# Kernel tuning notes

Measured on AMD Instinct MI355X. Metric: run time of the kernel, lower is better.

## Reference

```python
import jax, jax.numpy as jnp
import numpy as np

D_MODEL = 1024
N_HEADS = 16
HEAD_DIM = D_MODEL // N_HEADS
SCALE = float(np.sqrt(HEAD_DIM))


def setup_inputs() -> dict:
    key = jax.random.key(0)
    ks = jax.random.split(key, 12)
    B, S, D = 4, 2048, D_MODEL
    std = 1.0 / np.sqrt(D)
    inp = {
        "query": jax.random.normal(ks[0], (B, S, D), jnp.float32),
        "key": jax.random.normal(ks[1], (B, S, D), jnp.float32),
        "value": jax.random.normal(ks[2], (B, S, D), jnp.float32),
        "wq_w": jax.random.normal(ks[3], (D, D), jnp.float32) * std,
        "wq_b": jnp.zeros((D,), jnp.float32),
        "wk_w": jax.random.normal(ks[4], (D, D), jnp.float32) * std,
        "wk_b": jnp.zeros((D,), jnp.float32),
        "wv_w": jax.random.normal(ks[5], (D, D), jnp.float32) * std,
        "wv_b": jnp.zeros((D,), jnp.float32),
        "fc_w": jax.random.normal(ks[6], (D, D), jnp.float32) * std,
        "fc_b": jnp.zeros((D,), jnp.float32),
    }
    return inp


def reference(query, key, value, wq_w, wq_b, wk_w, wk_b, wv_w, wv_b, fc_w, fc_b):
    B, S, D = query.shape
    H, Hd = N_HEADS, HEAD_DIM
    # QKV projections (torch Linear: x @ W.T + b)
    Q = query @ wq_w.T + wq_b
    K = key @ wk_w.T + wk_b
    V = value @ wv_w.T + wv_b
    # [B, H, S, Hd]
    Q = Q.reshape(B, S, H, Hd).transpose(0, 2, 1, 3)
    K = K.reshape(B, S, H, Hd).transpose(0, 2, 1, 3)
    V = V.reshape(B, S, H, Hd).transpose(0, 2, 1, 3)
    energy = jnp.einsum("bhqd,bhkd->bhqk", Q, K) / SCALE
    attention = jax.nn.softmax(energy, axis=-1)  # dropout=0 (eval)
    weighted = jnp.einsum("bhqk,bhkd->bhqd", attention, V)
    weighted = weighted.transpose(0, 2, 1, 3).reshape(B, S, D)
    output = weighted @ fc_w.T + fc_b
    return (output, attention)
```

## Files before the change

kernel.cpp:

```cpp
#include <hip/hip_runtime.h>
#include <hip/hip_bf16.h>
#include <math.h>

typedef __attribute__((ext_vector_type(8))) short short8;
typedef __attribute__((ext_vector_type(4))) short short4v;
typedef __attribute__((ext_vector_type(4))) float float4v;
typedef __attribute__((ext_vector_type(2))) unsigned int uint2v;

#define GLD_LDS(g, l) __builtin_amdgcn_global_load_lds( \
    (const __attribute__((address_space(1))) void*)(g), \
    (__attribute__((address_space(3))) void*)(l), 16, 0, 0)

__device__ __forceinline__ short f2bf(float x) {
  __hip_bfloat16 h = __float2bfloat16(x);
  return __builtin_bit_cast(short, h);
}

__global__ __launch_bounds__(256) void cast3(
    const float4v* __restrict__ in0, const float4v* __restrict__ in1,
    const float4v* __restrict__ in2,
    short4v* __restrict__ o0, short4v* __restrict__ o1, short4v* __restrict__ o2,
    int n4)
{
  const float4v* in = blockIdx.y == 0 ? in0 : blockIdx.y == 1 ? in1 : in2;
  short4v* out = blockIdx.y == 0 ? o0 : blockIdx.y == 1 ? o1 : o2;
  int i = blockIdx.x * 256 + threadIdx.x;
  if (i < n4) {
    float4v v = in[i];
    short4v o;
    o[0] = f2bf(v[0]); o[1] = f2bf(v[1]); o[2] = f2bf(v[2]); o[3] = f2bf(v[3]);
    out[i] = o;
  }
}

__global__ __launch_bounds__(256) void cast4(
    const float4v* __restrict__ in0, const float4v* __restrict__ in1,
    const float4v* __restrict__ in2, const float4v* __restrict__ in3,
    short4v* __restrict__ o0, short4v* __restrict__ o1,
    short4v* __restrict__ o2, short4v* __restrict__ o3,
    int n4)
{
  const float4v* in = blockIdx.y == 0 ? in0 : blockIdx.y == 1 ? in1
                    : blockIdx.y == 2 ? in2 : in3;
  short4v* out = blockIdx.y == 0 ? o0 : blockIdx.y == 1 ? o1
               : blockIdx.y == 2 ? o2 : o3;
  int i = blockIdx.x * 256 + threadIdx.x;
  if (i < n4) {
    float4v v = in[i];
    short4v o;
    o[0] = f2bf(v[0]); o[1] = f2bf(v[1]); o[2] = f2bf(v[2]); o[3] = f2bf(v[3]);
    out[i] = o;
  }
}

template<int MODE>
__global__ __launch_bounds__(256) void gemm_bt(
    const short* __restrict__ A, const short* __restrict__ B,
    const float* __restrict__ bias, void* __restrict__ Cv,
    int M, int N, int K)
{
  __shared__ short As[2][128 * 64];
  __shared__ short Bs[2][128 * 64];
  const int tid = threadIdx.x;
  const int w = tid >> 6, lane = tid & 63;
  const int g = lane >> 4, cc = lane & 15;
  const int m0 = blockIdx.x * 128, n0 = blockIdx.y * 128;
  const int wr = (w >> 1) * 64, wc = (w & 1) * 64;

  float4v acc[4][4];
#pragma unroll
  for (int mi = 0; mi < 4; ++mi)
#pragma unroll
    for (int ni = 0; ni < 4; ++ni)
      acc[mi][ni] = (float4v){0.f, 0.f, 0.f, 0.f};

  const int cbase0 = w * 64;
  const int row_l[4] = {(cbase0 + lane) >> 3, (256 + cbase0 + lane) >> 3,
                        (512 + cbase0 + lane) >> 3, (768 + cbase0 + lane) >> 3};
  const int col_l = (lane & 7) * 8;

  auto stage = [&](int buf, int k0) {
#pragma unroll
    for (int i = 0; i < 4; ++i) {
      int cbase = i * 256 + cbase0;
      GLD_LDS(A + (long)(m0 + row_l[i]) * K + k0 + col_l, &As[buf][cbase * 8]);
      GLD_LDS(B + (long)(n0 + row_l[i]) * K + k0 + col_l, &Bs[buf][cbase * 8]);
    }
  };
  auto compute = [&](int buf) {
#pragma unroll
    for (int ks = 0; ks < 2; ++ks) {
      short8 af[4], bfr[4];
#pragma unroll
      for (int mi = 0; mi < 4; ++mi)
        af[mi] = *(const short8*)&As[buf][(wr + mi * 16 + cc) * 64 + ks * 32 + g * 8];
#pragma unroll
      for (int ni = 0; ni < 4; ++ni)
        bfr[ni] = *(const short8*)&Bs[buf][(wc + ni * 16 + cc) * 64 + ks * 32 + g * 8];
#pragma unroll
      for (int mi = 0; mi < 4; ++mi)
#pragma unroll
        for (int ni = 0; ni < 4; ++ni)
          acc[mi][ni] = __builtin_amdgcn_mfma_f32_16x16x32_bf16(
              af[mi], bfr[ni], acc[mi][ni], 0, 0, 0);
    }
  };

  stage(0, 0);
  __syncthreads();
#pragma unroll 1
  for (int k0 = 0; k0 < K; k0 += 128) {
    stage(1, k0 + 64);
    compute(0);
    __syncthreads();
    if (k0 + 128 < K) stage(0, k0 + 128);
    compute(1);
    __syncthreads();
  }

#pragma unroll
  for (int mi = 0; mi < 4; ++mi) {
#pragma unroll
    for (int ni = 0; ni < 4; ++ni) {
      int mb = m0 + wr + mi * 16 + g * 4;
      int nn = n0 + wc + ni * 16 + cc;
      float4v v = acc[mi][ni];
      if constexpr (MODE == 0) {
        float bb = bias[nn];
        __hip_bfloat16* C = (__hip_bfloat16*)Cv;
#pragma unroll
        for (int r = 0; r < 4; ++r)
          C[(long)(mb + r) * N + nn] = __float2bfloat16(v[r] + bb);
      } else if constexpr (MODE == 1) {
        __hip_bfloat16* C = (__hip_bfloat16*)Cv;
        long base = (long)(nn >> 11) * 2097152 + (nn & 2047);
#pragma unroll
        for (int r = 0; r < 4; ++r)
          C[(long)(mb + r) * 2048 + base] = __float2bfloat16(v[r] + bias[mb + r]);
      } else {
        float bb = bias[nn];
        float* C = (float*)Cv;
#pragma unroll
        for (int r = 0; r < 4; ++r)
          C[(long)(mb + r) * N + nn] = v[r] + bb;
      }
    }
  }
}

__global__ __launch_bounds__(256) void attn_fwd(
    const short* __restrict__ Qb, const short* __restrict__ Kb,
    const short* __restrict__ VTb, float* __restrict__ attn_out,
    __hip_bfloat16* __restrict__ Wout)
{
  __shared__ short plds[4][32][72];
  const int S = 2048, D = 1024;
  const int bid = blockIdx.x;
  const int x = bid >> 7, r = bid & 127;
  const int bh = x * 8 + (r & 7), qi = r >> 3;
  const int b = bh >> 4, h = bh & 15;
  const int tid = threadIdx.x, w = tid >> 6, lane = tid & 63;
  const int g = lane >> 4, cc = lane & 15;
  const int q0 = qi * 128 + w * 32;

  const short* Qp = Qb + (long)b * S * D + h * 64;
  const short* Kp = Kb + (long)b * S * D + h * 64;
  const short* Vt = VTb + (long)bh * 64 * S;

  short8 qf[2][2];
#pragma unroll
  for (int mi = 0; mi < 2; ++mi)
#pragma unroll
    for (int ks = 0; ks < 2; ++ks)
      qf[mi][ks] = *(const short8*)(Qp + (long)(q0 + mi * 16 + cc) * D + ks * 32 + g * 8);

  float l[2] = {0.f, 0.f};
  const float C2 = 0.18033688011112042f;

#pragma unroll 1
  for (int kt = 0; kt < S; kt += 64) {
    float4v e[2][4];
#pragma unroll
    for (int mi = 0; mi < 2; ++mi)
#pragma unroll
      for (int ni = 0; ni < 4; ++ni) e[mi][ni] = (float4v){0.f, 0.f, 0.f, 0.f};
#pragma unroll
    for (int ks = 0; ks < 2; ++ks) {
      short8 kf[4];
#pragma unroll
      for (int ni = 0; ni < 4; ++ni)
        kf[ni] = *(const short8*)(Kp + (long)(kt + ni * 16 + cc) * D + ks * 32 + g * 8);
#pragma unroll
      for (int mi = 0; mi < 2; ++mi)
#pragma unroll
        for (int ni = 0; ni < 4; ++ni)
          e[mi][ni] = __builtin_amdgcn_mfma_f32_16x16x32_bf16(
              kf[ni], qf[mi][ks], e[mi][ni], 0, 0, 0);
    }
#pragma unroll
    for (int mi = 0; mi < 2; ++mi)
#pragma unroll
      for (int ni = 0; ni < 4; ++ni)
#pragma unroll
        for (int r2 = 0; r2 < 4; ++r2)
          l[mi] += __builtin_exp2f(e[mi][ni][r2] * C2);
  }
  float lrl[2];
#pragma unroll
  for (int mi = 0; mi < 2; ++mi) {
    float s = l[mi];
    s += __shfl_xor(s, 16);
    s += __shfl_xor(s, 32);
    lrl[mi] = -__log2f(s);
  }

  float4v Wacc[2][4];
#pragma unroll
  for (int mi = 0; mi < 2; ++mi)
#pragma unroll
    for (int ni = 0; ni < 4; ++ni) Wacc[mi][ni] = (float4v){0.f, 0.f, 0.f, 0.f};

  float* Arow = attn_out + (long)bh * S * S;
#pragma unroll 1
  for (int kt = 0; kt < S; kt += 64) {
    float4v e[2][4];
#pragma unroll
    for (int mi = 0; mi < 2; ++mi)
#pragma unroll
      for (int ni = 0; ni < 4; ++ni) e[mi][ni] = (float4v){0.f, 0.f, 0.f, 0.f};
#pragma unroll
    for (int ks = 0; ks < 2; ++ks) {
      short8 kf[4];
#pragma unroll
      for (int ni = 0; ni < 4; ++ni)
        kf[ni] = *(const short8*)(Kp + (long)(kt + ni * 16 + cc) * D + ks * 32 + g * 8);
#pragma unroll
      for (int mi = 0; mi < 2; ++mi)
#pragma unroll
        for (int ni = 0; ni < 4; ++ni)
          e[mi][ni] = __builtin_amdgcn_mfma_f32_16x16x32_bf16(
              kf[ni], qf[mi][ks], e[mi][ni], 0, 0, 0);
    }
#pragma unroll
    for (int mi = 0; mi < 2; ++mi) {
#pragma unroll
      for (int ni = 0; ni < 4; ++ni) {
        short4v pb;
#pragma unroll
        for (int r2 = 0; r2 < 4; ++r2)
          pb[r2] = f2bf(__builtin_exp2f(__builtin_fmaf(e[mi][ni][r2], C2, lrl[mi])));
        *(short4v*)&plds[w][mi * 16 + cc][ni * 16 + g * 4] = pb;
      }
    }
#pragma unroll
    for (int j = 0; j < 8; ++j) {
      uint2v u = *(const uint2v*)&plds[w][j * 4 + g][cc * 4];
      float4v pv4;
      pv4[0] = __builtin_bit_cast(float, u[0] << 16);
      pv4[1] = __builtin_bit_cast(float, u[0] & 0xffff0000u);
      pv4[2] = __builtin_bit_cast(float, u[1] << 16);
      pv4[3] = __builtin_bit_cast(float, u[1] & 0xffff0000u);
      __builtin_nontemporal_store(
          pv4, (float4v*)(Arow + (long)(q0 + j * 4 + g) * S + kt + cc * 4));
    }
#pragma unroll
    for (int ks = 0; ks < 2; ++ks) {
      short8 pa[2], vf[4];
#pragma unroll
      for (int mi = 0; mi < 2; ++mi)
        pa[mi] = *(const short8*)&plds[w][mi * 16 + cc][ks * 32 + g * 8];
#pragma unroll
      for (int ni = 0; ni < 4; ++ni)
        vf[ni] = *(const short8*)(Vt + (long)(ni * 16 + cc) * S + kt + ks * 32 + g * 8);
#pragma unroll
      for (int mi = 0; mi < 2; ++mi)
#pragma unroll
        for (int ni = 0; ni < 4; ++ni)
          Wacc[mi][ni] = __builtin_amdgcn_mfma_f32_16x16x32_bf16(
              pa[mi], vf[ni], Wacc[mi][ni], 0, 0, 0);
    }
  }

#pragma unroll
  for (int mi = 0; mi < 2; ++mi)
#pragma unroll
    for (int ni = 0; ni < 4; ++ni)
#pragma unroll
      for (int r2 = 0; r2 < 4; ++r2)
        Wout[(long)(b * S + q0 + mi * 16 + g * 4 + r2) * D + h * 64 + ni * 16 + cc] =
            __float2bfloat16(Wacc[mi][ni][r2]);
}

extern "C" void kernel_launch(void* const* d_in, const int* in_sizes, int n_in,
                              void* d_out, int out_size, void* d_ws, size_t ws_size,
                              hipStream_t stream) {
  const float* query = (const float*)d_in[0];
  const float* key   = (const float*)d_in[1];
  const float* value = (const float*)d_in[2];
  const float* wq_w  = (const float*)d_in[3];
  const float* wq_b  = (const float*)d_in[4];
  const float* wk_w  = (const float*)d_in[5];
  const float* wk_b  = (const float*)d_in[6];
  const float* wv_w  = (const float*)d_in[7];
  const float* wv_b  = (const float*)d_in[8];
  const float* fc_w  = (const float*)d_in[9];
  const float* fc_b  = (const float*)d_in[10];

  char* ws = (char*)d_ws;
  short* Qb  = (short*)(ws);
  short* Kb  = (short*)(ws + 16777216);
  short* VT  = (short*)(ws + 33554432);
  short* Wq  = (short*)(ws + 50331648);
  short* Wk  = (short*)(ws + 52428800);
  short* Wv  = (short*)(ws + 54525952);
  short* Wfc = (short*)(ws + 56623104);
  short* Xq  = (short*)(ws + 58720256);
  short* Xk  = (short*)(ws + 75497472);
  short* Xv  = (short*)(ws + 92274688);
  short* Wgt = Xq;

  float* out0 = (float*)d_out;
  float* attn_out = out0 + 8388608;

  cast3<<<dim3(8192, 3), 256, 0, stream>>>(
      (const float4v*)query, (const float4v*)key, (const float4v*)value,
      (short4v*)Xq, (short4v*)Xk, (short4v*)Xv, 2097152);
  cast4<<<dim3(1024, 4), 256, 0, stream>>>(
      (const float4v*)wq_w, (const float4v*)wk_w, (const float4v*)wv_w,
      (const float4v*)fc_w,
      (short4v*)Wq, (short4v*)Wk, (short4v*)Wv, (short4v*)Wfc, 262144);

  gemm_bt<0><<<dim3(64, 8), 256, 0, stream>>>(Xq, Wq, wq_b, Qb, 8192, 1024, 1024);
  gemm_bt<0><<<dim3(64, 8), 256, 0, stream>>>(Xk, Wk, wk_b, Kb, 8192, 1024, 1024);
  gemm_bt<1><<<dim3(8, 64), 256, 0, stream>>>(Wv, Xv, wv_b, VT, 1024, 8192, 1024);

  attn_fwd<<<dim3(1024), 256, 0, stream>>>(Qb, Kb, VT, attn_out,
                                           (__hip_bfloat16*)Wgt);

  gemm_bt<2><<<dim3(64, 8), 256, 0, stream>>>(Wgt, Wfc, fc_b, out0, 8192, 1024, 1024);
}
```

Measured before the change: 543.0 us.

## Halve attention rows per wave to raise occupancy and parallelism

Each wave in the attention kernel now handles 16 query rows instead of 32, and each block covers 64 rows, so the grid grows to 2048 blocks laid out as (32,64). The block-to-head swizzle is dropped. Launch bounds now request 4 blocks per CU, the LDS tile is halved, and exp2 goes through the raw amdgcn intrinsic. Fewer registers per wave and more blocks are meant to hide memory latency on the large attention-matrix writes. In exchange, K and V are loaded twice as often per computed row, which reduces reuse and L2 locality across heads.

```diff
diff --git a/kernel.cpp b/kernel.cpp
--- a/kernel.cpp
+++ b/kernel.cpp
@@ -14,6 +14,10 @@
 __device__ __forceinline__ short f2bf(float x) {
   __hip_bfloat16 h = __float2bfloat16(x);
   return __builtin_bit_cast(short, h);
+}
+
+__device__ __forceinline__ float fexp2(float x) {
+  return __builtin_amdgcn_exp2f(x);
 }
 
 __global__ __launch_bounds__(256) void cast3(
@@ -148,112 +152,91 @@
   }
 }
 
-__global__ __launch_bounds__(256) void attn_fwd(
+__global__ __launch_bounds__(256, 4) void attn_fwd(
     const short* __restrict__ Qb, const short* __restrict__ Kb,
     const short* __restrict__ VTb, float* __restrict__ attn_out,
     __hip_bfloat16* __restrict__ Wout)
 {
-  __shared__ short plds[4][32][72];
+  __shared__ short plds[4][16][72];
   const int S = 2048, D = 1024;
-  const int bid = blockIdx.x;
-  const int x = bid >> 7, r = bid & 127;
-  const int bh = x * 8 + (r & 7), qi = r >> 3;
-  const int b = bh >> 4, h = bh & 15;
+  const int bh = blockIdx.y, b = bh >> 4, h = bh & 15;
   const int tid = threadIdx.x, w = tid >> 6, lane = tid & 63;
   const int g = lane >> 4, cc = lane & 15;
-  const int q0 = qi * 128 + w * 32;
+  const int q0 = blockIdx.x * 64 + w * 16;
 
   const short* Qp = Qb + (long)b * S * D + h * 64;
   const short* Kp = Kb + (long)b * S * D + h * 64;
   const short* Vt = VTb + (long)bh * 64 * S;
 
-  short8 qf[2][2];
-#pragma unroll
-  for (int mi = 0; mi < 2; ++mi)
-#pragma unroll
-    for (int ks = 0; ks < 2; ++ks)
-      qf[mi][ks] = *(const short8*)(Qp + (long)(q0 + mi * 16 + cc) * D + ks * 32 + g * 8);
-
-  float l[2] = {0.f, 0.f};
+  short8 qf[2];
+#pragma unroll
+  for (int ks = 0; ks < 2; ++ks)
+    qf[ks] = *(const short8*)(Qp + (long)(q0 + cc) * D + ks * 32 + g * 8);
+
+  float l = 0.f;
   const float C2 = 0.18033688011112042f;
 
 #pragma unroll 1
   for (int kt = 0; kt < S; kt += 64) {
-    float4v e[2][4];
-#pragma unroll
-    for (int mi = 0; mi < 2; ++mi)
-#pragma unroll
-      for (int ni = 0; ni < 4; ++ni) e[mi][ni] = (float4v){0.f, 0.f, 0.f, 0.f};
-#pragma unroll
-    for (int ks = 0; ks < 2; ++ks) {
-      short8 kf[4];
-#pragma unroll
-      for (int ni = 0; ni < 4; ++ni)
-        kf[ni] = *(const short8*)(Kp + (long)(kt + ni * 16 + cc) * D + ks * 32 + g * 8);
-#pragma unroll
-      for (int mi = 0; mi < 2; ++mi)
-#pragma unroll
-        for (int ni = 0; ni < 4; ++ni)
-          e[mi][ni] = __builtin_amdgcn_mfma_f32_16x16x32_bf16(
-              kf[ni], qf[mi][ks], e[mi][ni], 0, 0, 0);
-    }
-#pragma unroll
-    for (int mi = 0; mi < 2; ++mi)
-#pragma unroll
-      for (int ni = 0; ni < 4; ++ni)
-#pragma unroll
-        for (int r2 = 0; r2 < 4; ++r2)
-          l[mi] += __builtin_exp2f(e[mi][ni][r2] * C2);
-  }
-  float lrl[2];
-#pragma unroll
-  for (int mi = 0; mi < 2; ++mi) {
-    float s = l[mi];
-    s += __shfl_xor(s, 16);
-    s += __shfl_xor(s, 32);
-    lrl[mi] = -__log2f(s);
-  }
-
-  float4v Wacc[2][4];
-#pragma unroll
-  for (int mi = 0; mi < 2; ++mi)
-#pragma unroll
-    for (int ni = 0; ni < 4; ++ni) Wacc[mi][ni] = (float4v){0.f, 0.f, 0.f, 0.f};
+    short8 kf[2][4];
+#pragma unroll
+    for (int ks = 0; ks < 2; ++ks)
+#pragma unroll
+      for (int ni = 0; ni < 4; ++ni)
+        kf[ks][ni] = *(const short8*)(Kp + (long)(kt + ni * 16 + cc) * D + ks * 32 + g * 8);
+    float4v e[4];
+#pragma unroll
+    for (int ni = 0; ni < 4; ++ni) e[ni] = (float4v){0.f, 0.f, 0.f, 0.f};
+#pragma unroll
+    for (int ks = 0; ks < 2; ++ks)
+#pragma unroll
+      for (int ni = 0; ni < 4; ++ni)
+        e[ni] = __builtin_amdgcn_mfma_f32_16x16x32_bf16(
+            kf[ks][ni], qf[ks], e[ni], 0, 0, 0);
+#pragma unroll
+    for (int ni = 0; ni < 4; ++ni)
+#pragma unroll
+      for (int r2 = 0; r2 < 4; ++r2)
+        l += fexp2(e[ni][r2] * C2);
+  }
+  {
+    l += __shfl_xor(l, 16);
+    l += __shfl_xor(l, 32);
+  }
+  const float lrl = -__log2f(l);
+
+  float4v Wacc[4];
+#pragma unroll
+  for (int ni = 0; ni < 4; ++ni) Wacc[ni] = (float4v){0.f, 0.f, 0.f, 0.f};
 
   float* Arow = attn_out + (long)bh * S * S;
 #pragma unroll 1
   for (int kt = 0; kt < S; kt += 64) {
-    float4v e[2][4];
-#pragma unroll
-    for (int mi = 0; mi < 2; ++mi)
-#pragma unroll
-      for (int ni = 0; ni < 4; ++ni) e[mi][ni] = (float4v){0.f, 0.f, 0.f, 0.f};
-#pragma unroll
-    for (int ks = 0; ks < 2; ++ks) {
-      short8 kf[4];
-#pragma unroll
-      for (int ni = 0; ni < 4; ++ni)
-        kf[ni] = *(const short8*)(Kp + (long)(kt + ni * 16 + cc) * D + ks * 32 + g * 8);
-#pragma unroll
-      for (int mi = 0; mi < 2; ++mi)
-#pragma unroll
-        for (int ni = 0; ni < 4; ++ni)
-          e[mi][ni] = __builtin_amdgcn_mfma_f32_16x16x32_bf16(
-              kf[ni], qf[mi][ks], e[mi][ni], 0, 0, 0);
-    }
-#pragma unroll
-    for (int mi = 0; mi < 2; ++mi) {
-#pragma unroll
-      for (int ni = 0; ni < 4; ++ni) {
-        short4v pb;
-#pragma unroll
-        for (int r2 = 0; r2 < 4; ++r2)
-          pb[r2] = f2bf(__builtin_exp2f(__builtin_fmaf(e[mi][ni][r2], C2, lrl[mi])));
-        *(short4v*)&plds[w][mi * 16 + cc][ni * 16 + g * 4] = pb;
-      }
-    }
-#pragma unroll
-    for (int j = 0; j < 8; ++j) {
+    short8 kf[2][4];
+#pragma unroll
+    for (int ks = 0; ks < 2; ++ks)
+#pragma unroll
+      for (int ni = 0; ni < 4; ++ni)
+        kf[ks][ni] = *(const short8*)(Kp + (long)(kt + ni * 16 + cc) * D + ks * 32 + g * 8);
+    float4v e[4];
+#pragma unroll
+    for (int ni = 0; ni < 4; ++ni) e[ni] = (float4v){0.f, 0.f, 0.f, 0.f};
+#pragma unroll
+    for (int ks = 0; ks < 2; ++ks)
+#pragma unroll
+      for (int ni = 0; ni < 4; ++ni)
+        e[ni] = __builtin_amdgcn_mfma_f32_16x16x32_bf16(
+            kf[ks][ni], qf[ks], e[ni], 0, 0, 0);
+#pragma unroll
+    for (int ni = 0; ni < 4; ++ni) {
+      short4v pb;
+#pragma unroll
+      for (int r2 = 0; r2 < 4; ++r2)
+        pb[r2] = f2bf(fexp2(__builtin_fmaf(e[ni][r2], C2, lrl)));
+      *(short4v*)&plds[w][cc][ni * 16 + g * 4] = pb;
+    }
+#pragma unroll
+    for (int j = 0; j < 4; ++j) {
       uint2v u = *(const uint2v*)&plds[w][j * 4 + g][cc * 4];
       float4v pv4;
       pv4[0] = __builtin_bit_cast(float, u[0] << 16);
@@ -265,30 +248,21 @@
     }
 #pragma unroll
     for (int ks = 0; ks < 2; ++ks) {
-      short8 pa[2], vf[4];
-#pragma unroll
-      for (int mi = 0; mi < 2; ++mi)
-        pa[mi] = *(const short8*)&plds[w][mi * 16 + cc][ks * 32 + g * 8];
-#pragma unroll
-      for (int ni = 0; ni < 4; ++ni)
-        vf[ni] = *(const short8*)(Vt + (long)(ni * 16 + cc) * S + kt + ks * 32 + g * 8);
-#pragma unroll
-      for (int mi = 0; mi < 2; ++mi)
-#pragma unroll
-        for (int ni = 0; ni < 4; ++ni)
-          Wacc[mi][ni] = __builtin_amdgcn_mfma_f32_16x16x32_bf16(
-              pa[mi], vf[ni], Wacc[mi][ni], 0, 0, 0);
-    }
-  }
-
-#pragma unroll
-  for (int mi = 0; mi < 2; ++mi)
-#pragma unroll
-    for (int ni = 0; ni < 4; ++ni)
-#pragma unroll
-      for (int r2 = 0; r2 < 4; ++r2)
-        Wout[(long)(b * S + q0 + mi * 16 + g * 4 + r2) * D + h * 64 + ni * 16 + cc] =
-            __float2bfloat16(Wacc[mi][ni][r2]);
+      short8 pa = *(const short8*)&plds[w][cc][ks * 32 + g * 8];
+#pragma unroll
+      for (int ni = 0; ni < 4; ++ni) {
+        short8 vf = *(const short8*)(Vt + (long)(ni * 16 + cc) * S + kt + ks * 32 + g * 8);
+        Wacc[ni] = __builtin_amdgcn_mfma_f32_16x16x32_bf16(pa, vf, Wacc[ni], 0, 0, 0);
+      }
+    }
+  }
+
+#pragma unroll
+  for (int ni = 0; ni < 4; ++ni)
+#pragma unroll
+    for (int r2 = 0; r2 < 4; ++r2)
+      Wout[(long)(b * S + q0 + g * 4 + r2) * D + h * 64 + ni * 16 + cc] =
+          __float2bfloat16(Wacc[ni][r2]);
 }
 
 extern "C" void kernel_launch(void* const* d_in, const int* in_sizes, int n_in,
@@ -334,8 +308,8 @@
   gemm_bt<0><<<dim3(64, 8), 256, 0, stream>>>(Xk, Wk, wk_b, Kb, 8192, 1024, 1024);
   gemm_bt<1><<<dim3(8, 64), 256, 0, stream>>>(Wv, Xv, wv_b, VT, 1024, 8192, 1024);
 
-  attn_fwd<<<dim3(1024), 256, 0, stream>>>(Qb, Kb, VT, attn_out,
-                                           (__hip_bfloat16*)Wgt);
+  attn_fwd<<<dim3(32, 64), 256, 0, stream>>>(Qb, Kb, VT, attn_out,
+                                             (__hip_bfloat16*)Wgt);
 
   gemm_bt<2><<<dim3(64, 8), 256, 0, stream>>>(Wgt, Wfc, fc_b, out0, 8192, 1024, 1024);
 }
```

New measurement: 936.0 us. 72.4% more time.
